# Kernel tuning notes

Hardware: AMD Instinct MI355X
Metric: run time of the kernel (lower is better)

Reference implementation:

```python
import jax, jax.numpy as jnp
import numpy as np
from jax import lax

WBITS = 2
ABITS = 2
STRIDES = (1, 1)
PADDING = 'SAME'


def _ste_quantize(x, k):
    # round(x * n) / n with straight-through gradient (identity)
    n = float(2 ** k - 1)
    q = jnp.round(x * n) / n
    return x + lax.stop_gradient(q - x)


def _quantize_weight(w, k):
    # DoReFa-style weight quantization: tanh, normalize to [0,1], quantize, map to [-1,1]
    t = jnp.tanh(w)
    t = t / jnp.max(jnp.abs(t)) * 0.5 + 0.5
    return 2.0 * _ste_quantize(t, k) - 1.0


def _quantize_act(x, k):
    return _ste_quantize(jnp.clip(x, 0.0, 1.0), k)


def setup_inputs() -> dict:
    key = jax.random.key(0)
    kx, kw = jax.random.split(key)
    x = jax.random.uniform(kx, (32, 56, 56, 256), dtype=jnp.float32)  # NHWC
    w = jax.random.normal(kw, (3, 3, 256, 256), dtype=jnp.float32) * 0.2  # HWIO
    # match init normalization: unit L2 norm per output channel over (h,w,cin)
    w = w / jnp.sqrt(1e-7 + jnp.sum(w * w, axis=(0, 1, 2), keepdims=True))
    return {'x': x, 'w': w}


def reference(x, w) -> jnp.ndarray:
    wq = _quantize_weight(w, WBITS)        # low-bit weights in [-1, 1]
    xq = _quantize_act(x, ABITS)           # low-bit activations in [0, 1]
    out = lax.conv_general_dilated(
        xq, wq,
        window_strides=STRIDES,
        padding=PADDING,
        dimension_numbers=('NHWC', 'HWIO', 'NHWC'),
    )
    return out
```

## Files before the change

### kernel.cpp

```cpp
#include <hip/hip_runtime.h>
#include <stdint.h>

#define GLOBAL_AS __attribute__((address_space(1)))
#define LDS_AS    __attribute__((address_space(3)))

typedef int v4i  __attribute__((ext_vector_type(4)));
typedef int v16i __attribute__((ext_vector_type(16)));

__device__ __forceinline__ void gload_lds16(const void* g, void* l) {
    __builtin_amdgcn_global_load_lds((GLOBAL_AS uint32_t*)g, (LDS_AS uint32_t*)l, 16, 0, 0);
}

__global__ void k_xq_wmax(const float* __restrict__ x, const float* __restrict__ w,
                          int8_t* __restrict__ xqp, unsigned* __restrict__ maxbits) {
    const int bid = blockIdx.x;
    if (bid < 48) {
        int t = bid * 256 + threadIdx.x;
        const float4* w4 = (const float4*)w;
        float m = 0.f;
        for (int i = t; i < 147456; i += 12288) {
            float4 v = w4[i];
            m = fmaxf(m, fmaxf(fmaxf(fabsf(tanhf(v.x)), fabsf(tanhf(v.y))),
                               fmaxf(fabsf(tanhf(v.z)), fabsf(tanhf(v.w)))));
        }
#pragma unroll
        for (int off = 32; off > 0; off >>= 1)
            m = fmaxf(m, __shfl_xor(m, off, 64));
        if ((threadIdx.x & 63) == 0) atomicMax(maxbits, __float_as_uint(m));
        return;
    }
    int t = (bid - 48) * 256 + threadIdx.x;
    int g  = t & 15;
    int p  = t >> 4;
    int xp = p % 58;
    int q  = p / 58;
    int yp = q % 58;
    int n  = q / 58;
    int4 r;
    if (yp == 0 || yp == 57 || xp == 0 || xp == 57) {
        r = make_int4(0, 0, 0, 0);
    } else {
        const float4* px = (const float4*)(x + (((long)((n * 56 + (yp - 1)) * 56 + (xp - 1))) << 8) + g * 16);
        int wds[4];
#pragma unroll
        for (int jj = 0; jj < 4; ++jj) {
            float4 v = px[jj];
            int b0 = (int)rintf(fminf(fmaxf(v.x, 0.f), 1.f) * 3.f);
            int b1 = (int)rintf(fminf(fmaxf(v.y, 0.f), 1.f) * 3.f);
            int b2 = (int)rintf(fminf(fmaxf(v.z, 0.f), 1.f) * 3.f);
            int b3 = (int)rintf(fminf(fmaxf(v.w, 0.f), 1.f) * 3.f);
            wds[jj] = b0 | (b1 << 8) | (b2 << 16) | (b3 << 24);
        }
        r = make_int4(wds[0], wds[1], wds[2], wds[3]);
    }
    *(int4*)(xqp + ((long)t << 4)) = r;
}

__global__ void k_wq(const float* __restrict__ w, const unsigned* __restrict__ maxbits,
                     int8_t* __restrict__ wqt) {
    int t = blockIdx.x * 256 + threadIdx.x;
    int co = t & 255;
    int kblk = t >> 8;
    float inv = 0.5f / __uint_as_float(*maxbits);
    int8_t b[16];
#pragma unroll
    for (int i = 0; i < 16; ++i) {
        float tv = tanhf(w[(long)(kblk * 16 + i) * 256 + co]);
        int qi = (int)rintf((tv * inv + 0.5f) * 3.0f);
        b[i] = (int8_t)(2 * qi - 3);
    }
    *(int4*)(wqt + (long)co * 2304 + kblk * 16) = *(int4*)b;
}

#define BM 128
#define BN 128

__global__ __launch_bounds__(256) void k_conv(const int8_t* __restrict__ xqp,
                                              const int8_t* __restrict__ wqt,
                                              float* __restrict__ out) {
    __shared__ int8_t sA[2][BM * 128];
    __shared__ int8_t sB[2][BN * 128];

    const int tid    = threadIdx.x;
    const int wv     = tid >> 6;
    const int lane   = tid & 63;
    const int orig   = blockIdx.x;
    const int work   = (orig & 7) * 196 + (orig >> 3);
    const int coBase = (work & 1) * BN;
    const int mBase  = (work >> 1) * BM;

    const int lr = lane >> 3;
    const int lp = lane & 7;
    const int8_t* aB[4];
    const int8_t* bB[4];
#pragma unroll
    for (int j = 0; j < 4; ++j) {
        int r = wv * 8 + j * 32 + lr;
        int g = lp ^ (r & 7);
        int m = mBase + r;
        int n = m / 3136;
        int rem = m - n * 3136;
        int y = rem / 56;
        int x = rem - y * 56;
        aB[j] = xqp + (((long)((n * 58 + y) * 58 + x)) << 8) + g * 16;
        bB[j] = wqt + (long)(coBase + r) * 2304 + g * 16;
    }

    v16i acc[2][2];
#pragma unroll
    for (int a = 0; a < 2; ++a)
#pragma unroll
        for (int b = 0; b < 2; ++b)
#pragma unroll
            for (int r = 0; r < 16; ++r) acc[a][b][r] = 0;

    const int wm  = (wv & 1) * 64;
    const int wn  = (wv >> 1) * 64;
    const int l31 = lane & 31;
    const int hi  = lane >> 5;

    const int rA0 = (wm + l31) * 128;       const int axr0 = ((wm + l31) & 7) << 4;
    const int rA1 = (wm + 32 + l31) * 128;  const int axr1 = ((wm + 32 + l31) & 7) << 4;
    const int rB0 = (wn + l31) * 128;       const int bxr0 = ((wn + l31) & 7) << 4;
    const int rB1 = (wn + 32 + l31) * 128;  const int bxr1 = ((wn + 32 + l31) & 7) << 4;

    auto issue = [&](int it, int b) {
        int tap = it >> 1;
        int ky  = tap / 3;
        int kx  = tap - ky * 3;
        int aOff = ((ky * 58 + kx) << 8) + (it & 1) * 128;
        int bOff = tap * 256 + (it & 1) * 128;
#pragma unroll
        for (int j = 0; j < 4; ++j) {
            gload_lds16(aB[j] + aOff, &sA[b][(wv * 8 + j * 32) * 128]);
            gload_lds16(bB[j] + bOff, &sB[b][(wv * 8 + j * 32) * 128]);
        }
    };

    auto compute = [&](int b) {
        const int8_t* pA = sA[b];
        const int8_t* pB = sB[b];
        __builtin_amdgcn_s_setprio(1);
#pragma unroll
        for (int kk = 0; kk < 4; ++kk) {
            const int kc = (kk * 2 + hi) << 4;
            v4i a0 = *(const v4i*)(pA + rA0 + (kc ^ axr0));
            v4i a1 = *(const v4i*)(pA + rA1 + (kc ^ axr1));
            v4i b0 = *(const v4i*)(pB + rB0 + (kc ^ bxr0));
            v4i b1 = *(const v4i*)(pB + rB1 + (kc ^ bxr1));
            acc[0][0] = __builtin_amdgcn_mfma_i32_32x32x32_i8(a0, b0, acc[0][0], 0, 0, 0);
            acc[0][1] = __builtin_amdgcn_mfma_i32_32x32x32_i8(a0, b1, acc[0][1], 0, 0, 0);
            acc[1][0] = __builtin_amdgcn_mfma_i32_32x32x32_i8(a1, b0, acc[1][0], 0, 0, 0);
            acc[1][1] = __builtin_amdgcn_mfma_i32_32x32x32_i8(a1, b1, acc[1][1], 0, 0, 0);
        }
        __builtin_amdgcn_s_setprio(0);
    };

    issue(0, 0);
#pragma unroll 2
    for (int it = 0; it < 17; ++it) {
        issue(it + 1, (it + 1) & 1);
        asm volatile("s_waitcnt vmcnt(8)" ::: "memory");
        __builtin_amdgcn_s_barrier();
        asm volatile("" ::: "memory");
        compute(it & 1);
        asm volatile("" ::: "memory");
        __builtin_amdgcn_s_barrier();
        asm volatile("" ::: "memory");
    }
    asm volatile("s_waitcnt vmcnt(0)" ::: "memory");
    __builtin_amdgcn_s_barrier();
    asm volatile("" ::: "memory");
    compute(1);

    const float s = 1.0f / 9.0f;
#pragma unroll
    for (int mt = 0; mt < 2; ++mt) {
#pragma unroll
        for (int nt = 0; nt < 2; ++nt) {
            const int ocol = coBase + wn + nt * 32 + l31;
#pragma unroll
            for (int reg = 0; reg < 16; ++reg) {
                const int row = (reg & 3) + 8 * (reg >> 2) + 4 * hi;
                const long orow = mBase + wm + mt * 32 + row;
                out[orow * 256 + ocol] = (float)acc[mt][nt][reg] * s;
            }
        }
    }
}

extern "C" void kernel_launch(void* const* d_in, const int* in_sizes, int n_in,
                              void* d_out, int out_size, void* d_ws, size_t ws_size,
                              hipStream_t stream) {
    const float* x = (const float*)d_in[0];
    const float* w = (const float*)d_in[1];
    float* out = (float*)d_out;

    unsigned* maxbits = (unsigned*)d_ws;
    int8_t* wqt = (int8_t*)d_ws + 4096;
    int8_t* xqp = (int8_t*)d_ws + 4096 + 589824;

    hipMemsetAsync(maxbits, 0, 4, stream);
    k_xq_wmax<<<48 + 6728, 256, 0, stream>>>(x, w, xqp, maxbits);
    k_wq<<<144, 256, 0, stream>>>(w, maxbits, wqt);
    k_conv<<<1568, 256, 0, stream>>>(xqp, wqt, out);
}
```

Before: 254.3 us.

## Pack activations and weights as FP4 and use scaled f8f6f4 MFMA

Activations (0..3) and weights (-3,-1,1,3) are encoded as 4-bit FP4 (e2m1) nibbles, two values per byte. The workspace shrinks by half, and the conv inner loop now runs 9 K-steps of 64 through the MX-scaled 32x32x64 f8f6f4 MFMA with fp32 accumulation, replacing 18 int8 MFMA steps. The aims are to halve the global/LDS traffic for the packed operands and to use the FP4 matrix rate. The risk is exactness: it relies on every quantized value being representable in e2m1 with unit scale (0x7F exponent), and on the half-zero v8i operand packing matching what the instruction expects for FP4.

```diff
diff --git a/kernel.cpp b/kernel.cpp
--- a/kernel.cpp
+++ b/kernel.cpp
@@ -4,12 +4,14 @@
 #define GLOBAL_AS __attribute__((address_space(1)))
 #define LDS_AS    __attribute__((address_space(3)))
 
-typedef int v4i  __attribute__((ext_vector_type(4)));
-typedef int v16i __attribute__((ext_vector_type(16)));
+typedef int   v4i  __attribute__((ext_vector_type(4)));
+typedef int   v8i  __attribute__((ext_vector_type(8)));
+typedef float v16f __attribute__((ext_vector_type(16)));
 
 __device__ __forceinline__ void gload_lds16(const void* g, void* l) {
     __builtin_amdgcn_global_load_lds((GLOBAL_AS uint32_t*)g, (LDS_AS uint32_t*)l, 16, 0, 0);
 }
+
 
 __global__ void k_xq_wmax(const float* __restrict__ x, const float* __restrict__ w,
                           int8_t* __restrict__ xqp, unsigned* __restrict__ maxbits) {
@@ -30,8 +32,8 @@
         return;
     }
     int t = (bid - 48) * 256 + threadIdx.x;
-    int g  = t & 15;
-    int p  = t >> 4;
+    int g  = t & 7;
+    int p  = t >> 3;
     int xp = p % 58;
     int q  = p / 58;
     int yp = q % 58;
@@ -40,16 +42,24 @@
     if (yp == 0 || yp == 57 || xp == 0 || xp == 57) {
         r = make_int4(0, 0, 0, 0);
     } else {
-        const float4* px = (const float4*)(x + (((long)((n * 56 + (yp - 1)) * 56 + (xp - 1))) << 8) + g * 16);
+        const float4* px = (const float4*)(x + (((long)((n * 56 + (yp - 1)) * 56 + (xp - 1))) << 8) + g * 32);
         int wds[4];
 #pragma unroll
         for (int jj = 0; jj < 4; ++jj) {
-            float4 v = px[jj];
-            int b0 = (int)rintf(fminf(fmaxf(v.x, 0.f), 1.f) * 3.f);
-            int b1 = (int)rintf(fminf(fmaxf(v.y, 0.f), 1.f) * 3.f);
-            int b2 = (int)rintf(fminf(fmaxf(v.z, 0.f), 1.f) * 3.f);
-            int b3 = (int)rintf(fminf(fmaxf(v.w, 0.f), 1.f) * 3.f);
-            wds[jj] = b0 | (b1 << 8) | (b2 << 16) | (b3 << 24);
+            float4 v0 = px[jj * 2];
+            float4 v1 = px[jj * 2 + 1];
+            int q0 = (int)rintf(fminf(fmaxf(v0.x, 0.f), 1.f) * 3.f);
+            int q1 = (int)rintf(fminf(fmaxf(v0.y, 0.f), 1.f) * 3.f);
+            int q2 = (int)rintf(fminf(fmaxf(v0.z, 0.f), 1.f) * 3.f);
+            int q3 = (int)rintf(fminf(fmaxf(v0.w, 0.f), 1.f) * 3.f);
+            int q4 = (int)rintf(fminf(fmaxf(v1.x, 0.f), 1.f) * 3.f);
+            int q5 = (int)rintf(fminf(fmaxf(v1.y, 0.f), 1.f) * 3.f);
+            int q6 = (int)rintf(fminf(fmaxf(v1.z, 0.f), 1.f) * 3.f);
+            int q7 = (int)rintf(fminf(fmaxf(v1.w, 0.f), 1.f) * 3.f);
+            wds[jj] = ((0x5420 >> (q0 << 2)) & 0xF)        | (((0x5420 >> (q1 << 2)) & 0xF) << 4)
+                    | (((0x5420 >> (q2 << 2)) & 0xF) << 8) | (((0x5420 >> (q3 << 2)) & 0xF) << 12)
+                    | (((0x5420 >> (q4 << 2)) & 0xF) << 16)| (((0x5420 >> (q5 << 2)) & 0xF) << 20)
+                    | (((0x5420 >> (q6 << 2)) & 0xF) << 24)| (((0x5420 >> (q7 << 2)) & 0xF) << 28);
         }
         r = make_int4(wds[0], wds[1], wds[2], wds[3]);
     }
@@ -62,14 +72,16 @@
     int co = t & 255;
     int kblk = t >> 8;
     float inv = 0.5f / __uint_as_float(*maxbits);
-    int8_t b[16];
-#pragma unroll
-    for (int i = 0; i < 16; ++i) {
-        float tv = tanhf(w[(long)(kblk * 16 + i) * 256 + co]);
-        int qi = (int)rintf((tv * inv + 0.5f) * 3.0f);
-        b[i] = (int8_t)(2 * qi - 3);
-    }
-    *(int4*)(wqt + (long)co * 2304 + kblk * 16) = *(int4*)b;
+    uint8_t b[16];
+#pragma unroll
+    for (int j = 0; j < 16; ++j) {
+        float t0 = tanhf(w[(long)(kblk * 32 + 2 * j) * 256 + co]);
+        float t1 = tanhf(w[(long)(kblk * 32 + 2 * j + 1) * 256 + co]);
+        int q0 = (int)rintf((t0 * inv + 0.5f) * 3.0f);
+        int q1 = (int)rintf((t1 * inv + 0.5f) * 3.0f);
+        b[j] = (uint8_t)(((0x52AD >> (q0 << 2)) & 0xF) | (((0x52AD >> (q1 << 2)) & 0xF) << 4));
+    }
+    *(int4*)(wqt + (long)co * 1152 + kblk * 16) = *(int4*)b;
 }
 
 #define BM 128
@@ -102,17 +114,17 @@
         int rem = m - n * 3136;
         int y = rem / 56;
         int x = rem - y * 56;
-        aB[j] = xqp + (((long)((n * 58 + y) * 58 + x)) << 8) + g * 16;
-        bB[j] = wqt + (long)(coBase + r) * 2304 + g * 16;
-    }
-
-    v16i acc[2][2];
+        aB[j] = xqp + (((long)((n * 58 + y) * 58 + x)) << 7) + g * 16;
+        bB[j] = wqt + (long)(coBase + r) * 1152 + g * 16;
+    }
+
+    v16f acc[2][2];
 #pragma unroll
     for (int a = 0; a < 2; ++a)
 #pragma unroll
         for (int b = 0; b < 2; ++b)
 #pragma unroll
-            for (int r = 0; r < 16; ++r) acc[a][b][r] = 0;
+            for (int r = 0; r < 16; ++r) acc[a][b][r] = 0.f;
 
     const int wm  = (wv & 1) * 64;
     const int wn  = (wv >> 1) * 64;
@@ -125,17 +137,18 @@
     const int rB1 = (wn + 32 + l31) * 128;  const int bxr1 = ((wn + 32 + l31) & 7) << 4;
 
     auto issue = [&](int it, int b) {
-        int tap = it >> 1;
-        int ky  = tap / 3;
-        int kx  = tap - ky * 3;
-        int aOff = ((ky * 58 + kx) << 8) + (it & 1) * 128;
-        int bOff = tap * 256 + (it & 1) * 128;
+        int ky  = it / 3;
+        int kx  = it - ky * 3;
+        int aOff = (ky * 58 + kx) << 7;
+        int bOff = it << 7;
 #pragma unroll
         for (int j = 0; j < 4; ++j) {
             gload_lds16(aB[j] + aOff, &sA[b][(wv * 8 + j * 32) * 128]);
             gload_lds16(bB[j] + bOff, &sB[b][(wv * 8 + j * 32) * 128]);
         }
     };
+
+    const int SC = 0x7F7F7F7F;
 
     auto compute = [&](int b) {
         const int8_t* pA = sA[b];
@@ -148,17 +161,21 @@
             v4i a1 = *(const v4i*)(pA + rA1 + (kc ^ axr1));
             v4i b0 = *(const v4i*)(pB + rB0 + (kc ^ bxr0));
             v4i b1 = *(const v4i*)(pB + rB1 + (kc ^ bxr1));
-            acc[0][0] = __builtin_amdgcn_mfma_i32_32x32x32_i8(a0, b0, acc[0][0], 0, 0, 0);
-            acc[0][1] = __builtin_amdgcn_mfma_i32_32x32x32_i8(a0, b1, acc[0][1], 0, 0, 0);
-            acc[1][0] = __builtin_amdgcn_mfma_i32_32x32x32_i8(a1, b0, acc[1][0], 0, 0, 0);
-            acc[1][1] = __builtin_amdgcn_mfma_i32_32x32x32_i8(a1, b1, acc[1][1], 0, 0, 0);
+            v8i A0 = {a0[0], a0[1], a0[2], a0[3], 0, 0, 0, 0};
+            v8i A1 = {a1[0], a1[1], a1[2], a1[3], 0, 0, 0, 0};
+            v8i B0 = {b0[0], b0[1], b0[2], b0[3], 0, 0, 0, 0};
+            v8i B1 = {b1[0], b1[1], b1[2], b1[3], 0, 0, 0, 0};
+            acc[0][0] = __builtin_amdgcn_mfma_scale_f32_32x32x64_f8f6f4(A0, B0, acc[0][0], 4, 4, 0, SC, 0, SC);
+            acc[0][1] = __builtin_amdgcn_mfma_scale_f32_32x32x64_f8f6f4(A0, B1, acc[0][1], 4, 4, 0, SC, 0, SC);
+            acc[1][0] = __builtin_amdgcn_mfma_scale_f32_32x32x64_f8f6f4(A1, B0, acc[1][0], 4, 4, 0, SC, 0, SC);
+            acc[1][1] = __builtin_amdgcn_mfma_scale_f32_32x32x64_f8f6f4(A1, B1, acc[1][1], 4, 4, 0, SC, 0, SC);
         }
         __builtin_amdgcn_s_setprio(0);
     };
 
     issue(0, 0);
 #pragma unroll 2
-    for (int it = 0; it < 17; ++it) {
+    for (int it = 0; it < 8; ++it) {
         issue(it + 1, (it + 1) & 1);
         asm volatile("s_waitcnt vmcnt(8)" ::: "memory");
         __builtin_amdgcn_s_barrier();
@@ -171,7 +188,7 @@
     asm volatile("s_waitcnt vmcnt(0)" ::: "memory");
     __builtin_amdgcn_s_barrier();
     asm volatile("" ::: "memory");
-    compute(1);
+    compute(0);
 
     const float s = 1.0f / 9.0f;
 #pragma unroll
@@ -183,7 +200,7 @@
             for (int reg = 0; reg < 16; ++reg) {
                 const int row = (reg & 3) + 8 * (reg >> 2) + 4 * hi;
                 const long orow = mBase + wm + mt * 32 + row;
-                out[orow * 256 + ocol] = (float)acc[mt][nt][reg] * s;
+                out[orow * 256 + ocol] = acc[mt][nt][reg] * s;
             }
         }
     }
@@ -198,10 +215,10 @@
 
     unsigned* maxbits = (unsigned*)d_ws;
     int8_t* wqt = (int8_t*)d_ws + 4096;
-    int8_t* xqp = (int8_t*)d_ws + 4096 + 589824;
+    int8_t* xqp = (int8_t*)d_ws + 4096 + 294912;
 
     hipMemsetAsync(maxbits, 0, 4, stream);
-    k_xq_wmax<<<48 + 6728, 256, 0, stream>>>(x, w, xqp, maxbits);
-    k_wq<<<144, 256, 0, stream>>>(w, maxbits, wqt);
+    k_xq_wmax<<<48 + 3364, 256, 0, stream>>>(x, w, xqp, maxbits);
+    k_wq<<<72, 256, 0, stream>>>(w, maxbits, wqt);
     k_conv<<<1568, 256, 0, stream>>>(xqp, wqt, out);
 }
```

Result: faster. 229.7 us (-9.7%).
